# Performance work log

Hardware: AMD Instinct MI355X
Metric: run time of the kernel (lower is better)

Reference implementation:

```python
import jax, jax.numpy as jnp
import numpy as np

H, HKV, D = 16, 4, 64
ROPE_BASE = 10000.0
EPS = 1e-6


def _rms_norm(x):
    return x * jax.lax.rsqrt(jnp.mean(x * x, axis=-1, keepdims=True) + EPS)


def _rope_cos_sin(T, dtype):
    inv_freq = 1.0 / (ROPE_BASE ** (jnp.arange(0, D, 2, dtype=jnp.float32) / D))  # [D/2]
    t = jnp.arange(T, dtype=jnp.float32)
    freqs = jnp.outer(t, inv_freq)  # [T, D/2]
    return jnp.cos(freqs)[None, :, None, :].astype(dtype), jnp.sin(freqs)[None, :, None, :].astype(dtype)


def _apply_rope(x, cos, sin):
    d = x.shape[-1] // 2
    x1, x2 = x[..., :d], x[..., d:]
    return jnp.concatenate([x1 * cos + x2 * sin, -x1 * sin + x2 * cos], axis=-1)


def setup_inputs() -> dict:
    key = jax.random.key(0)
    ks = jax.random.split(key, 6)
    B, T, dm = 1, 2048, 1024
    x = jax.random.normal(ks[0], (B, T, dm), dtype=jnp.float32)
    q_w = jax.random.normal(ks[1], (H * D, dm), dtype=jnp.float32) * 0.02
    k_w = jax.random.normal(ks[2], (HKV * D, dm), dtype=jnp.float32) * 0.02
    v_w = jax.random.normal(ks[3], (HKV * D, dm), dtype=jnp.float32) * 0.02
    o_w = jax.random.normal(ks[4], (dm, H * D), dtype=jnp.float32) * 0.02
    temp = jnp.ones((H,), dtype=jnp.float32) * np.sqrt(D)  # per-head temperature buffer
    curvature = jnp.asarray(1.0, dtype=jnp.float32)
    return {"x": x, "q_w": q_w, "k_w": k_w, "v_w": v_w, "o_w": o_w, "temp": temp, "curvature": curvature}


def reference(x, q_w, k_w, v_w, o_w, temp, curvature):
    B, T, dm = x.shape
    # projections
    q = (x @ q_w.T).reshape(B, T, H, D)
    k = (x @ k_w.T).reshape(B, T, HKV, D)
    v = (x @ v_w.T).reshape(B, T, HKV, D)
    q, k = _rms_norm(q), _rms_norm(k)
    cos, sin = _rope_cos_sin(T, q.dtype)
    q = _apply_rope(q, cos, sin)
    k = _apply_rope(k, cos, sin)
    # GQA: repeat kv heads
    rep = H // HKV
    k = jnp.repeat(k, rep, axis=2)  # [B,T,H,D]
    v = jnp.repeat(v, rep, axis=2)
    c = curvature
    # hyperboloid lift: time component x0 = sqrt(1/c + ||x||^2)
    q0 = jnp.sqrt(1.0 / c + jnp.sum(q * q, axis=-1))  # [B,T,H]
    k0 = jnp.sqrt(1.0 / c + jnp.sum(k * k, axis=-1))
    # Minkowski inner product <q,k>_L = q.k_spatial - q0*k0  -> [B,H,Tq,Tk]
    mink = jnp.einsum('bqhd,bkhd->bhqk', q, k) - q0.transpose(0, 2, 1)[..., :, None] * k0.transpose(0, 2, 1)[..., None, :]
    # Lorentz distance d = arccosh(clamp(-c*<q,k>_L, 1+eps)) / sqrt(c)
    dist = jnp.arccosh(jnp.maximum(-c * mink, 1.0 + 1e-5)) / jnp.sqrt(c)
    scores = -dist / temp[None, :, None, None]
    causal = jnp.tril(jnp.ones((T, T), dtype=bool))
    scores = jnp.where(causal[None, None], scores, -jnp.inf)
    w = jax.nn.softmax(scores, axis=-1)  # [B,H,Tq,Tk]
    attn = jnp.einsum('bhqk,bkhd->bqhd', w, v).reshape(B, T, H * D)
    out = attn @ o_w.T  # [B,T,dm]
    spatial_norm = jnp.mean(jnp.sqrt(jnp.sum(q * q, axis=-1)))
    return out, spatial_norm
```

## Files before the change

kernel.cpp:

```cpp
#include <hip/hip_runtime.h>
#include <hip/hip_bf16.h>

typedef __attribute__((ext_vector_type(8))) short short8;
typedef __attribute__((ext_vector_type(4))) short bf16x4;
typedef __attribute__((ext_vector_type(4))) float f32x4;

#define TT 2048
#define DM 1024
#define NH 16
#define NKV 4
#define HD 64

#define MFMA32(a,b,c) __builtin_amdgcn_mfma_f32_16x16x32_bf16(a,b,c,0,0,0)
#define MFMA16(a,b,c) __builtin_amdgcn_mfma_f32_16x16x16bf16_1k(a,b,c,0,0,0)

__device__ __forceinline__ unsigned short f2bf(float x){
  unsigned int u = __float_as_uint(x);
  u += 0x7fffu + ((u >> 16) & 1u);
  return (unsigned short)(u >> 16);
}
__device__ __forceinline__ unsigned int pkbf2(float x, float y){
  union { __hip_bfloat162 h; unsigned int u; } t;
  t.h = __float22bfloat162_rn(make_float2(x, y));
  return t.u;
}
__device__ __forceinline__ void gl_lds16(const unsigned short* g, unsigned short* l){
  __builtin_amdgcn_global_load_lds(
      (__attribute__((address_space(1))) void*)g,
      (__attribute__((address_space(3))) void*)l, 16, 0, 0);
}

__global__ __launch_bounds__(256) void convertw_kernel(
    const float* __restrict__ x,
    const float* __restrict__ qw, const float* __restrict__ kw,
    const float* __restrict__ vw, const float* __restrict__ ow,
    unsigned short* __restrict__ xb,
    unsigned short* __restrict__ wqkv, unsigned short* __restrict__ owb){
  long v = (long)blockIdx.x * 256 + threadIdx.x;
  const float* src; unsigned short* dst; long base;
  if      (v < 524288) { src = x;  dst = xb;             base = v; }
  else if (v < 786432) { src = qw; dst = wqkv;           base = v - 524288; }
  else if (v < 851968) { src = kw; dst = wqkv + 1048576; base = v - 786432; }
  else if (v < 917504) { src = vw; dst = wqkv + 1310720; base = v - 851968; }
  else                 { src = ow; dst = owb;            base = v - 917504; }
  f32x4 d = *(const f32x4*)(src + base * 4);
  uint2 pk = { pkbf2(d[0], d[1]), pkbf2(d[2], d[3]) };
  *(uint2*)(dst + base * 4) = pk;
}

__global__ __launch_bounds__(256) void gemm1_fused(
    const unsigned short* __restrict__ xb, const unsigned short* __restrict__ wqkv,
    unsigned short* __restrict__ qb, unsigned short* __restrict__ kb,
    unsigned short* __restrict__ vt,
    float* __restrict__ q0, float* __restrict__ k0,
    float* __restrict__ bpart, const float* __restrict__ curv){
  __shared__ __align__(16) unsigned short As[2 * 64 * 32];
  __shared__ __align__(16) unsigned short Bs[2 * 64 * 32];
  __shared__ float Ct[64 * 65];
  __shared__ float bsum;
  const int tid = threadIdx.x, lane = tid & 63, wave = tid >> 6;
  const int hIdx = blockIdx.x;
  const int bm = blockIdx.y * 64, bn = hIdx * 64;
  const int wm = (wave >> 1) * 32, wn = (wave & 1) * 32;
  const int ml = lane & 15, quad = lane >> 4;
  if (tid == 0) bsum = 0.f;
  f32x4 acc[2][2];
  const f32x4 z = {0.f, 0.f, 0.f, 0.f};
  acc[0][0] = z; acc[0][1] = z; acc[1][0] = z; acc[1][1] = z;

  const int srow = wave * 16 + (lane >> 2), scol = (lane & 3) * 8;
  const unsigned short* Ag = xb   + (long)(bm + srow) * 1024 + scol;
  const unsigned short* Bg = wqkv + (long)(bn + srow) * 1024 + scol;
  unsigned short* Al0 = As + wave * 512;
  unsigned short* Al1 = As + 2048 + wave * 512;
  unsigned short* Bl0 = Bs + wave * 512;
  unsigned short* Bl1 = Bs + 2048 + wave * 512;

  for (int kk = 0; kk < 1024; kk += 64){
    __syncthreads();
    gl_lds16(Ag + kk,      Al0);
    gl_lds16(Ag + kk + 32, Al1);
    gl_lds16(Bg + kk,      Bl0);
    gl_lds16(Bg + kk + 32, Bl1);
    __syncthreads();
#pragma unroll
    for (int half = 0; half < 2; half++){
      const unsigned short* Ah = As + half * 2048;
      const unsigned short* Bh = Bs + half * 2048;
      short8 a0f = *(const short8*)&Ah[(wm + ml) * 32 + quad * 8];
      short8 a1f = *(const short8*)&Ah[(wm + 16 + ml) * 32 + quad * 8];
      short8 b0f = *(const short8*)&Bh[(wn + ml) * 32 + quad * 8];
      short8 b1f = *(const short8*)&Bh[(wn + 16 + ml) * 32 + quad * 8];
      acc[0][0] = MFMA32(a0f, b0f, acc[0][0]);
      acc[0][1] = MFMA32(a0f, b1f, acc[0][1]);
      acc[1][0] = MFMA32(a1f, b0f, acc[1][0]);
      acc[1][1] = MFMA32(a1f, b1f, acc[1][1]);
    }
  }
  __syncthreads();
#pragma unroll
  for (int i = 0; i < 2; i++)
#pragma unroll
    for (int j = 0; j < 2; j++)
#pragma unroll
      for (int r = 0; r < 4; r++)
        Ct[(wm + i * 16 + quad * 4 + r) * 65 + wn + j * 16 + ml] = acc[i][j][r];
  __syncthreads();

  if (hIdx < 20){
    const bool isq = hIdx < 16;
    const int h = isq ? hIdx : hIdx - 16;
    const float c = curv[0];
    unsigned short* ob = isq ? qb : kb;
    float* o0 = isq ? q0 : k0;
#pragma unroll 1
    for (int rr = 0; rr < 16; rr++){
      const int row = wave * 16 + rr;
      const int t = bm + row;
      float val = Ct[row * 65 + lane];
      float ss = val * val;
#pragma unroll
      for (int off = 1; off < 64; off <<= 1) ss += __shfl_xor(ss, off);
      float scale = __builtin_amdgcn_rsqf(ss * (1.f / 64.f) + 1e-6f);
      float xn = val * scale;
      float other = __shfl_xor(xn, 32);
      int fi = lane & 31;
      float ang = (float)t * __builtin_amdgcn_exp2f((float)fi * (-13.287712379549449f / 32.f));
      float sn, cs; __sincosf(ang, &sn, &cs);
      float outv = (lane < 32) ? (xn * cs + other * sn) : (xn * cs - other * sn);
      ob[((long)h * TT + t) * 64 + lane] = f2bf(outv);
      if (lane == 0){
        float sq = ss * scale * scale;
        o0[h * TT + t] = __builtin_amdgcn_sqrtf(1.f / c + sq);
        if (isq) atomicAdd(&bsum, __builtin_amdgcn_sqrtf(sq));
      }
    }
  } else {
    const int hk = hIdx - 20;
    const int d = tid >> 2, tseg = (tid & 3) * 16;
    uint4 w0, w1;
    w0.x = pkbf2(Ct[(tseg + 0) * 65 + d], Ct[(tseg + 1) * 65 + d]);
    w0.y = pkbf2(Ct[(tseg + 2) * 65 + d], Ct[(tseg + 3) * 65 + d]);
    w0.z = pkbf2(Ct[(tseg + 4) * 65 + d], Ct[(tseg + 5) * 65 + d]);
    w0.w = pkbf2(Ct[(tseg + 6) * 65 + d], Ct[(tseg + 7) * 65 + d]);
    w1.x = pkbf2(Ct[(tseg + 8) * 65 + d], Ct[(tseg + 9) * 65 + d]);
    w1.y = pkbf2(Ct[(tseg +10) * 65 + d], Ct[(tseg +11) * 65 + d]);
    w1.z = pkbf2(Ct[(tseg +12) * 65 + d], Ct[(tseg +13) * 65 + d]);
    w1.w = pkbf2(Ct[(tseg +14) * 65 + d], Ct[(tseg +15) * 65 + d]);
    const int tile = (bm + tseg) >> 4;
    unsigned short* dst = vt + ((long)(hk * 128 + tile) * 64 + d) * 16;
    *(uint4*)dst = w0;
    *(uint4*)(dst + 8) = w1;
  }
  __syncthreads();
  if (tid == 0) bpart[blockIdx.y * 24 + hIdx] = bsum;
}

__global__ __launch_bounds__(256, 3) void attn_kernel(
    const unsigned short* __restrict__ qb_, const unsigned short* __restrict__ kb_,
    const unsigned short* __restrict__ vt_,
    const float* __restrict__ q0_, const float* __restrict__ k0_,
    const float* __restrict__ temp, const float* __restrict__ curv,
    unsigned short* __restrict__ attn_out,
    const float* __restrict__ bpart, float* __restrict__ out_scalar){
  __shared__ float lds[8 * 1104];
  const int tid = threadIdx.x, lane = tid & 63, wave = tid >> 6;
  const int qt  = 127 - (blockIdx.x >> 3);
  const int sub = blockIdx.x & 7;
  const int kvh = sub >> 1, hp = sub & 1;
  const int h0 = kvh * 4 + hp * 2, h1 = h0 + 1;
  const int i0 = qt * 16;
  const int ml = lane & 15, quad = lane >> 4;
  const float c = curv[0];
  const float rsc = __builtin_amdgcn_rsqf(c);
  const float fac0 = -rsc / temp[h0];
  const float fac1 = -rsc / temp[h1];
  const f32x4 z = {0.f, 0.f, 0.f, 0.f};
  const unsigned short* kh = kb_ + (long)kvh * TT * 64;
  const unsigned short* vh = vt_ + (long)kvh * 128 * 1024;
  const float* k0h = k0_ + kvh * TT;

  short8 qa0 = *(const short8*)&qb_[((long)h0 * TT + i0 + ml) * 64 + quad * 8];
  short8 qa1 = *(const short8*)&qb_[((long)h0 * TT + i0 + ml) * 64 + 32 + quad * 8];
  short8 qb0 = *(const short8*)&qb_[((long)h1 * TT + i0 + ml) * 64 + quad * 8];
  short8 qb1 = *(const short8*)&qb_[((long)h1 * TT + i0 + ml) * 64 + 32 + quad * 8];
  const float q0c0 = c * q0_[h0 * TT + i0 + ml];
  const float q0c1 = c * q0_[h1 * TT + i0 + ml];
  const int rowq = i0 + ml;

  f32x4 o0[4], o1[4];
#pragma unroll
  for (int dt = 0; dt < 4; dt++){ o0[dt] = z; o1[dt] = z; }
  float l0 = 0.f, l1 = 0.f;

  const int nt = (i0 + 47) >> 5;

#pragma unroll 1
  for (int t = wave; t < nt; t += 4){
    const int j0 = t << 5;
    const unsigned short* kp = kh + (long)j0 * 64;
    short8 ka0 = *(const short8*)(kp + ml * 64 + quad * 8);
    short8 ka1 = *(const short8*)(kp + ml * 64 + 32 + quad * 8);
    short8 kc0 = *(const short8*)(kp + (16 + ml) * 64 + quad * 8);
    short8 kc1 = *(const short8*)(kp + (16 + ml) * 64 + 32 + quad * 8);
    f32x4 k0a = *(const f32x4*)(k0h + j0 + quad * 4);
    f32x4 k0b = *(const f32x4*)(k0h + j0 + 16 + quad * 4);
    const unsigned short* vpa = vh + (long)(j0 >> 4) * 1024;
    bf16x4 vfa0 = *(const bf16x4*)(vpa + ( 0 + ml) * 16 + quad * 4);
    bf16x4 vfa1 = *(const bf16x4*)(vpa + (16 + ml) * 16 + quad * 4);
    bf16x4 vfa2 = *(const bf16x4*)(vpa + (32 + ml) * 16 + quad * 4);
    bf16x4 vfa3 = *(const bf16x4*)(vpa + (48 + ml) * 16 + quad * 4);
    bf16x4 vfb0 = *(const bf16x4*)(vpa + 1024 + ( 0 + ml) * 16 + quad * 4);
    bf16x4 vfb1 = *(const bf16x4*)(vpa + 1024 + (16 + ml) * 16 + quad * 4);
    bf16x4 vfb2 = *(const bf16x4*)(vpa + 1024 + (32 + ml) * 16 + quad * 4);
    bf16x4 vfb3 = *(const bf16x4*)(vpa + 1024 + (48 + ml) * 16 + quad * 4);

    const int keyb = j0 + quad * 4;
    const bool nm = (j0 + 31 > i0);
    {
      f32x4 s0 = z, s1 = z;
      s0 = MFMA32(ka0, qa0, s0);
      s0 = MFMA32(ka1, qa1, s0);
      s1 = MFMA32(kc0, qa0, s1);
      s1 = MFMA32(kc1, qa1, s1);
      float p0[4], p1[4];
#pragma unroll
      for (int r = 0; r < 4; r++){
        float argA = fmaxf(__builtin_fmaf(-c, s0[r], q0c0 * k0a[r]), 1.00001f);
        float wA   = argA + __builtin_amdgcn_sqrtf(__builtin_fmaf(argA, argA, -1.f));
        float pA   = __builtin_amdgcn_exp2f(fac0 * __builtin_amdgcn_logf(wA));
        float argB = fmaxf(__builtin_fmaf(-c, s1[r], q0c0 * k0b[r]), 1.00001f);
        float wB   = argB + __builtin_amdgcn_sqrtf(__builtin_fmaf(argB, argB, -1.f));
        float pB   = __builtin_amdgcn_exp2f(fac0 * __builtin_amdgcn_logf(wB));
        if (nm){
          if (keyb + r > rowq)      pA = 0.f;
          if (keyb + 16 + r > rowq) pB = 0.f;
        }
        p0[r] = pA; p1[r] = pB;
        l0 += pA + pB;
      }
      uint2 pua = { pkbf2(p0[0], p0[1]), pkbf2(p0[2], p0[3]) };
      uint2 pub = { pkbf2(p1[0], p1[1]), pkbf2(p1[2], p1[3]) };
      bf16x4 pfa = *(bf16x4*)&pua;
      bf16x4 pfb = *(bf16x4*)&pub;
      o0[0] = MFMA16(vfa0, pfa, o0[0]);
      o0[1] = MFMA16(vfa1, pfa, o0[1]);
      o0[2] = MFMA16(vfa2, pfa, o0[2]);
      o0[3] = MFMA16(vfa3, pfa, o0[3]);
      o0[0] = MFMA16(vfb0, pfb, o0[0]);
      o0[1] = MFMA16(vfb1, pfb, o0[1]);
      o0[2] = MFMA16(vfb2, pfb, o0[2]);
      o0[3] = MFMA16(vfb3, pfb, o0[3]);
    }
    {
      f32x4 s0 = z, s1 = z;
      s0 = MFMA32(ka0, qb0, s0);
      s0 = MFMA32(ka1, qb1, s0);
      s1 = MFMA32(kc0, qb0, s1);
      s1 = MFMA32(kc1, qb1, s1);
      float p0[4], p1[4];
#pragma unroll
      for (int r = 0; r < 4; r++){
        float argA = fmaxf(__builtin_fmaf(-c, s0[r], q0c1 * k0a[r]), 1.00001f);
        float wA   = argA + __builtin_amdgcn_sqrtf(__builtin_fmaf(argA, argA, -1.f));
        float pA   = __builtin_amdgcn_exp2f(fac1 * __builtin_amdgcn_logf(wA));
        float argB = fmaxf(__builtin_fmaf(-c, s1[r], q0c1 * k0b[r]), 1.00001f);
        float wB   = argB + __builtin_amdgcn_sqrtf(__builtin_fmaf(argB, argB, -1.f));
        float pB   = __builtin_amdgcn_exp2f(fac1 * __builtin_amdgcn_logf(wB));
        if (nm){
          if (keyb + r > rowq)      pA = 0.f;
          if (keyb + 16 + r > rowq) pB = 0.f;
        }
        p0[r] = pA; p1[r] = pB;
        l1 += pA + pB;
      }
      uint2 pua = { pkbf2(p0[0], p0[1]), pkbf2(p0[2], p0[3]) };
      uint2 pub = { pkbf2(p1[0], p1[1]), pkbf2(p1[2], p1[3]) };
      bf16x4 pfa = *(bf16x4*)&pua;
      bf16x4 pfb = *(bf16x4*)&pub;
      o1[0] = MFMA16(vfa0, pfa, o1[0]);
      o1[1] = MFMA16(vfa1, pfa, o1[1]);
      o1[2] = MFMA16(vfa2, pfa, o1[2]);
      o1[3] = MFMA16(vfa3, pfa, o1[3]);
      o1[0] = MFMA16(vfb0, pfb, o1[0]);
      o1[1] = MFMA16(vfb1, pfb, o1[1]);
      o1[2] = MFMA16(vfb2, pfb, o1[2]);
      o1[3] = MFMA16(vfb3, pfb, o1[3]);
    }
  }
  l0 += __shfl_xor(l0, 16); l0 += __shfl_xor(l0, 32);
  l1 += __shfl_xor(l1, 16); l1 += __shfl_xor(l1, 32);
  {
    float* w0 = lds + wave * 1104;
    float* w1 = lds + (4 + wave) * 1104;
#pragma unroll
    for (int dt = 0; dt < 4; dt++){
      *(f32x4*)&w0[ml * 68 + dt * 16 + quad * 4] = o0[dt];
      *(f32x4*)&w1[ml * 68 + dt * 16 + quad * 4] = o1[dt];
    }
    if (quad == 0){ w0[1088 + ml] = l0; w1[1088 + ml] = l1; }
  }
  __syncthreads();
  {
    const int row = tid >> 4, c0 = (tid & 15) * 4;
#pragma unroll 1
    for (int hb = 0; hb < 2; hb++){
      const float* base = lds + hb * 4 * 1104;
      float L = 0.f; f32x4 s = z;
#pragma unroll
      for (int w = 0; w < 4; w++){
        const float* rg = base + w * 1104;
        L += rg[1088 + row];
        f32x4 t2 = *(const f32x4*)&rg[row * 68 + c0];
        s[0] += t2[0]; s[1] += t2[1]; s[2] += t2[2]; s[3] += t2[3];
      }
      float invL = __builtin_amdgcn_rcpf(L);
      const int h = hb ? h1 : h0;
      uint2 o = { pkbf2(s[0] * invL, s[1] * invL), pkbf2(s[2] * invL, s[3] * invL) };
      *(uint2*)&attn_out[(long)(i0 + row) * 1024 + h * 64 + c0] = o;
    }
  }
  if (blockIdx.x == 0 && tid < 64){
    float s = 0.f;
    for (int i = lane; i < 768; i += 64) s += bpart[i];
#pragma unroll
    for (int off = 1; off < 64; off <<= 1) s += __shfl_xor(s, off);
    if (lane == 0) out_scalar[0] = s * (1.f / 32768.f);
  }
}

__global__ __launch_bounds__(256) void gemm2_kernel(
    const unsigned short* __restrict__ A, const unsigned short* __restrict__ B,
    float* __restrict__ C){
  __shared__ __align__(16) unsigned short As[2 * 64 * 32];
  __shared__ __align__(16) unsigned short Bs[2 * 64 * 32];
  const int tid = threadIdx.x, lane = tid & 63, wave = tid >> 6;
  const int bm = blockIdx.y * 64, bn = blockIdx.x * 64;
  const int wm = (wave >> 1) * 32, wn = (wave & 1) * 32;
  const int ml = lane & 15, quad = lane >> 4;
  f32x4 acc[2][2];
  const f32x4 z = {0.f, 0.f, 0.f, 0.f};
  acc[0][0] = z; acc[0][1] = z; acc[1][0] = z; acc[1][1] = z;

  const int srow = wave * 16 + (lane >> 2), scol = (lane & 3) * 8;
  const unsigned short* Ag = A + (long)(bm + srow) * 1024 + scol;
  const unsigned short* Bg = B + (long)(bn + srow) * 1024 + scol;
  unsigned short* Al0 = As + wave * 512;
  unsigned short* Al1 = As + 2048 + wave * 512;
  unsigned short* Bl0 = Bs + wave * 512;
  unsigned short* Bl1 = Bs + 2048 + wave * 512;

  for (int kk = 0; kk < 1024; kk += 64){
    __syncthreads();
    gl_lds16(Ag + kk,      Al0);
    gl_lds16(Ag + kk + 32, Al1);
    gl_lds16(Bg + kk,      Bl0);
    gl_lds16(Bg + kk + 32, Bl1);
    __syncthreads();
#pragma unroll
    for (int half = 0; half < 2; half++){
      const unsigned short* Ah = As + half * 2048;
      const unsigned short* Bh = Bs + half * 2048;
      short8 a0f = *(const short8*)&Ah[(wm + ml) * 32 + quad * 8];
      short8 a1f = *(const short8*)&Ah[(wm + 16 + ml) * 32 + quad * 8];
      short8 b0f = *(const short8*)&Bh[(wn + ml) * 32 + quad * 8];
      short8 b1f = *(const short8*)&Bh[(wn + 16 + ml) * 32 + quad * 8];
      acc[0][0] = MFMA32(a0f, b0f, acc[0][0]);
      acc[0][1] = MFMA32(a0f, b1f, acc[0][1]);
      acc[1][0] = MFMA32(a1f, b0f, acc[1][0]);
      acc[1][1] = MFMA32(a1f, b1f, acc[1][1]);
    }
  }
#pragma unroll
  for (int i = 0; i < 2; i++)
#pragma unroll
    for (int j = 0; j < 2; j++)
#pragma unroll
      for (int r = 0; r < 4; r++)
        C[(long)(bm + wm + i * 16 + quad * 4 + r) * 1024 + bn + wn + j * 16 + ml] = acc[i][j][r];
}

extern "C" void kernel_launch(void* const* d_in, const int* in_sizes, int n_in,
                              void* d_out, int out_size, void* d_ws, size_t ws_size,
                              hipStream_t stream){
  const float* x    = (const float*)d_in[0];
  const float* qw   = (const float*)d_in[1];
  const float* kw   = (const float*)d_in[2];
  const float* vw   = (const float*)d_in[3];
  const float* ow   = (const float*)d_in[4];
  const float* temp = (const float*)d_in[5];
  const float* curv = (const float*)d_in[6];
  float* out = (float*)d_out;

  char* ws = (char*)d_ws;
  size_t off = 0;
  auto alloc = [&](size_t bytes) -> char* {
    char* p = ws + off;
    off += (bytes + 255) & ~(size_t)255;
    return p;
  };
  unsigned short* xb   = (unsigned short*)alloc((size_t)TT * DM * 2);
  unsigned short* wqkv = (unsigned short*)alloc((size_t)1536 * DM * 2);
  unsigned short* owb  = (unsigned short*)alloc((size_t)DM * DM * 2);
  unsigned short* qb   = (unsigned short*)alloc((size_t)NH * TT * HD * 2);
  unsigned short* kb   = (unsigned short*)alloc((size_t)NKV * TT * HD * 2);
  unsigned short* vt   = (unsigned short*)alloc((size_t)NKV * TT * HD * 2);
  float*          q0   = (float*)alloc((size_t)NH * TT * 4);
  float*          k0   = (float*)alloc((size_t)NKV * TT * 4);
  unsigned short* attn = (unsigned short*)alloc((size_t)TT * DM * 2);
  float*          bpart= (float*)alloc((size_t)768 * 4);

  convertw_kernel<<<4608, 256, 0, stream>>>(x, qw, kw, vw, ow, xb, wqkv, owb);
  gemm1_fused<<<dim3(24, 32), 256, 0, stream>>>(xb, wqkv, qb, kb, vt, q0, k0, bpart, curv);
  attn_kernel<<<1024, 256, 0, stream>>>(qb, kb, vt, q0, k0, temp, curv, attn,
                                        bpart, out + (size_t)TT * DM);
  gemm2_kernel<<<dim3(16, 32), 256, 0, stream>>>(attn, owb, out);
}
```

Measured before the change: 144.5 us.

## Enlarge GEMM block tiles to 128x64 and alias epilogue LDS with staging buffers

Both projection GEMMs now compute a 128x64 output tile per block, with each wave owning 32 rows by 64 columns (2x4 MFMA accumulators) instead of a 32x32 quadrant. The aim is more MFMA work per LDS fragment load and fewer blocks, which halves the grid, reduces reloading of the B tile, and raises arithmetic intensity. In gemm1 the epilogue transpose buffer shares LDS with the operand staging buffers so the larger tile fits. The trade-off is fewer blocks (384 and 256) across the GPU's compute units and more registers per thread, with the partial-sum buffer for the scalar norm resized to match.

```diff
diff --git a/kernel.cpp b/kernel.cpp
--- a/kernel.cpp
+++ b/kernel.cpp
@@ -54,57 +54,67 @@
     unsigned short* __restrict__ vt,
     float* __restrict__ q0, float* __restrict__ k0,
     float* __restrict__ bpart, const float* __restrict__ curv){
-  __shared__ __align__(16) unsigned short As[2 * 64 * 32];
-  __shared__ __align__(16) unsigned short Bs[2 * 64 * 32];
-  __shared__ float Ct[64 * 65];
+  __shared__ __align__(16) char smem[33280];
+  unsigned short* As = (unsigned short*)smem;
+  unsigned short* Bs = As + 8192;
+  float* Ct = (float*)smem;
   __shared__ float bsum;
   const int tid = threadIdx.x, lane = tid & 63, wave = tid >> 6;
   const int hIdx = blockIdx.x;
-  const int bm = blockIdx.y * 64, bn = hIdx * 64;
-  const int wm = (wave >> 1) * 32, wn = (wave & 1) * 32;
+  const int bm = blockIdx.y * 128, bn = hIdx * 64;
+  const int wm = wave * 32;
   const int ml = lane & 15, quad = lane >> 4;
   if (tid == 0) bsum = 0.f;
-  f32x4 acc[2][2];
+  f32x4 acc[2][4];
   const f32x4 z = {0.f, 0.f, 0.f, 0.f};
-  acc[0][0] = z; acc[0][1] = z; acc[1][0] = z; acc[1][1] = z;
-
-  const int srow = wave * 16 + (lane >> 2), scol = (lane & 3) * 8;
-  const unsigned short* Ag = xb   + (long)(bm + srow) * 1024 + scol;
-  const unsigned short* Bg = wqkv + (long)(bn + srow) * 1024 + scol;
-  unsigned short* Al0 = As + wave * 512;
-  unsigned short* Al1 = As + 2048 + wave * 512;
-  unsigned short* Bl0 = Bs + wave * 512;
-  unsigned short* Bl1 = Bs + 2048 + wave * 512;
+#pragma unroll
+  for (int i = 0; i < 2; i++)
+#pragma unroll
+    for (int j = 0; j < 4; j++) acc[i][j] = z;
+
+  const int lrow = lane >> 2, lcol = (lane & 3) * 8;
+  const unsigned short* AgW = xb   + (long)(bm + wm + lrow) * 1024 + lcol;
+  const unsigned short* BgW = wqkv + (long)(bn + wave * 16 + lrow) * 1024 + lcol;
+  unsigned short* AdW = As + wave * 1024;
+  unsigned short* BdW = Bs + wave * 512;
 
   for (int kk = 0; kk < 1024; kk += 64){
     __syncthreads();
-    gl_lds16(Ag + kk,      Al0);
-    gl_lds16(Ag + kk + 32, Al1);
-    gl_lds16(Bg + kk,      Bl0);
-    gl_lds16(Bg + kk + 32, Bl1);
+#pragma unroll
+    for (int h = 0; h < 2; h++){
+      gl_lds16(AgW + kk + h * 32,            AdW + h * 4096);
+      gl_lds16(AgW + 16384 + kk + h * 32,    AdW + h * 4096 + 512);
+      gl_lds16(BgW + kk + h * 32,            BdW + h * 2048);
+    }
     __syncthreads();
 #pragma unroll
-    for (int half = 0; half < 2; half++){
-      const unsigned short* Ah = As + half * 2048;
-      const unsigned short* Bh = Bs + half * 2048;
+    for (int h = 0; h < 2; h++){
+      const unsigned short* Ah = As + h * 4096;
+      const unsigned short* Bh = Bs + h * 2048;
       short8 a0f = *(const short8*)&Ah[(wm + ml) * 32 + quad * 8];
       short8 a1f = *(const short8*)&Ah[(wm + 16 + ml) * 32 + quad * 8];
-      short8 b0f = *(const short8*)&Bh[(wn + ml) * 32 + quad * 8];
-      short8 b1f = *(const short8*)&Bh[(wn + 16 + ml) * 32 + quad * 8];
+      short8 b0f = *(const short8*)&Bh[(     ml) * 32 + quad * 8];
+      short8 b1f = *(const short8*)&Bh[(16 + ml) * 32 + quad * 8];
+      short8 b2f = *(const short8*)&Bh[(32 + ml) * 32 + quad * 8];
+      short8 b3f = *(const short8*)&Bh[(48 + ml) * 32 + quad * 8];
       acc[0][0] = MFMA32(a0f, b0f, acc[0][0]);
       acc[0][1] = MFMA32(a0f, b1f, acc[0][1]);
+      acc[0][2] = MFMA32(a0f, b2f, acc[0][2]);
+      acc[0][3] = MFMA32(a0f, b3f, acc[0][3]);
       acc[1][0] = MFMA32(a1f, b0f, acc[1][0]);
       acc[1][1] = MFMA32(a1f, b1f, acc[1][1]);
+      acc[1][2] = MFMA32(a1f, b2f, acc[1][2]);
+      acc[1][3] = MFMA32(a1f, b3f, acc[1][3]);
     }
   }
   __syncthreads();
 #pragma unroll
   for (int i = 0; i < 2; i++)
 #pragma unroll
-    for (int j = 0; j < 2; j++)
+    for (int j = 0; j < 4; j++)
 #pragma unroll
       for (int r = 0; r < 4; r++)
-        Ct[(wm + i * 16 + quad * 4 + r) * 65 + wn + j * 16 + ml] = acc[i][j][r];
+        Ct[(wm + i * 16 + quad * 4 + r) * 65 + j * 16 + ml] = acc[i][j][r];
   __syncthreads();
 
   if (hIdx < 20){
@@ -114,8 +124,8 @@
     unsigned short* ob = isq ? qb : kb;
     float* o0 = isq ? q0 : k0;
 #pragma unroll 1
-    for (int rr = 0; rr < 16; rr++){
-      const int row = wave * 16 + rr;
+    for (int rr = 0; rr < 32; rr++){
+      const int row = wave * 32 + rr;
       const int t = bm + row;
       float val = Ct[row * 65 + lane];
       float ss = val * val;
@@ -137,20 +147,24 @@
     }
   } else {
     const int hk = hIdx - 20;
-    const int d = tid >> 2, tseg = (tid & 3) * 16;
-    uint4 w0, w1;
-    w0.x = pkbf2(Ct[(tseg + 0) * 65 + d], Ct[(tseg + 1) * 65 + d]);
-    w0.y = pkbf2(Ct[(tseg + 2) * 65 + d], Ct[(tseg + 3) * 65 + d]);
-    w0.z = pkbf2(Ct[(tseg + 4) * 65 + d], Ct[(tseg + 5) * 65 + d]);
-    w0.w = pkbf2(Ct[(tseg + 6) * 65 + d], Ct[(tseg + 7) * 65 + d]);
-    w1.x = pkbf2(Ct[(tseg + 8) * 65 + d], Ct[(tseg + 9) * 65 + d]);
-    w1.y = pkbf2(Ct[(tseg +10) * 65 + d], Ct[(tseg +11) * 65 + d]);
-    w1.z = pkbf2(Ct[(tseg +12) * 65 + d], Ct[(tseg +13) * 65 + d]);
-    w1.w = pkbf2(Ct[(tseg +14) * 65 + d], Ct[(tseg +15) * 65 + d]);
-    const int tile = (bm + tseg) >> 4;
-    unsigned short* dst = vt + ((long)(hk * 128 + tile) * 64 + d) * 16;
-    *(uint4*)dst = w0;
-    *(uint4*)(dst + 8) = w1;
+    const int d = tid >> 2;
+#pragma unroll
+    for (int half = 0; half < 2; half++){
+      const int tseg = (tid & 3) * 16 + half * 64;
+      uint4 w0, w1;
+      w0.x = pkbf2(Ct[(tseg + 0) * 65 + d], Ct[(tseg + 1) * 65 + d]);
+      w0.y = pkbf2(Ct[(tseg + 2) * 65 + d], Ct[(tseg + 3) * 65 + d]);
+      w0.z = pkbf2(Ct[(tseg + 4) * 65 + d], Ct[(tseg + 5) * 65 + d]);
+      w0.w = pkbf2(Ct[(tseg + 6) * 65 + d], Ct[(tseg + 7) * 65 + d]);
+      w1.x = pkbf2(Ct[(tseg + 8) * 65 + d], Ct[(tseg + 9) * 65 + d]);
+      w1.y = pkbf2(Ct[(tseg +10) * 65 + d], Ct[(tseg +11) * 65 + d]);
+      w1.z = pkbf2(Ct[(tseg +12) * 65 + d], Ct[(tseg +13) * 65 + d]);
+      w1.w = pkbf2(Ct[(tseg +14) * 65 + d], Ct[(tseg +15) * 65 + d]);
+      const int tile = (bm + tseg) >> 4;
+      unsigned short* dst = vt + ((long)(hk * 128 + tile) * 64 + d) * 16;
+      *(uint4*)dst = w0;
+      *(uint4*)(dst + 8) = w1;
+    }
   }
   __syncthreads();
   if (tid == 0) bpart[blockIdx.y * 24 + hIdx] = bsum;
@@ -322,7 +336,7 @@
   }
   if (blockIdx.x == 0 && tid < 64){
     float s = 0.f;
-    for (int i = lane; i < 768; i += 64) s += bpart[i];
+    for (int i = lane; i < 384; i += 64) s += bpart[i];
 #pragma unroll
     for (int off = 1; off < 64; off <<= 1) s += __shfl_xor(s, off);
     if (lane == 0) out_scalar[0] = s * (1.f / 32768.f);
@@ -332,52 +346,61 @@
 __global__ __launch_bounds__(256) void gemm2_kernel(
     const unsigned short* __restrict__ A, const unsigned short* __restrict__ B,
     float* __restrict__ C){
-  __shared__ __align__(16) unsigned short As[2 * 64 * 32];
+  __shared__ __align__(16) unsigned short As[2 * 128 * 32];
   __shared__ __align__(16) unsigned short Bs[2 * 64 * 32];
   const int tid = threadIdx.x, lane = tid & 63, wave = tid >> 6;
-  const int bm = blockIdx.y * 64, bn = blockIdx.x * 64;
-  const int wm = (wave >> 1) * 32, wn = (wave & 1) * 32;
+  const int bm = blockIdx.y * 128, bn = blockIdx.x * 64;
+  const int wm = wave * 32;
   const int ml = lane & 15, quad = lane >> 4;
-  f32x4 acc[2][2];
+  f32x4 acc[2][4];
   const f32x4 z = {0.f, 0.f, 0.f, 0.f};
-  acc[0][0] = z; acc[0][1] = z; acc[1][0] = z; acc[1][1] = z;
-
-  const int srow = wave * 16 + (lane >> 2), scol = (lane & 3) * 8;
-  const unsigned short* Ag = A + (long)(bm + srow) * 1024 + scol;
-  const unsigned short* Bg = B + (long)(bn + srow) * 1024 + scol;
-  unsigned short* Al0 = As + wave * 512;
-  unsigned short* Al1 = As + 2048 + wave * 512;
-  unsigned short* Bl0 = Bs + wave * 512;
-  unsigned short* Bl1 = Bs + 2048 + wave * 512;
+#pragma unroll
+  for (int i = 0; i < 2; i++)
+#pragma unroll
+    for (int j = 0; j < 4; j++) acc[i][j] = z;
+
+  const int lrow = lane >> 2, lcol = (lane & 3) * 8;
+  const unsigned short* AgW = A + (long)(bm + wm + lrow) * 1024 + lcol;
+  const unsigned short* BgW = B + (long)(bn + wave * 16 + lrow) * 1024 + lcol;
+  unsigned short* AdW = As + wave * 1024;
+  unsigned short* BdW = Bs + wave * 512;
 
   for (int kk = 0; kk < 1024; kk += 64){
     __syncthreads();
-    gl_lds16(Ag + kk,      Al0);
-    gl_lds16(Ag + kk + 32, Al1);
-    gl_lds16(Bg + kk,      Bl0);
-    gl_lds16(Bg + kk + 32, Bl1);
+#pragma unroll
+    for (int h = 0; h < 2; h++){
+      gl_lds16(AgW + kk + h * 32,         AdW + h * 4096);
+      gl_lds16(AgW + 16384 + kk + h * 32, AdW + h * 4096 + 512);
+      gl_lds16(BgW + kk + h * 32,         BdW + h * 2048);
+    }
     __syncthreads();
 #pragma unroll
-    for (int half = 0; half < 2; half++){
-      const unsigned short* Ah = As + half * 2048;
-      const unsigned short* Bh = Bs + half * 2048;
+    for (int h = 0; h < 2; h++){
+      const unsigned short* Ah = As + h * 4096;
+      const unsigned short* Bh = Bs + h * 2048;
       short8 a0f = *(const short8*)&Ah[(wm + ml) * 32 + quad * 8];
       short8 a1f = *(const short8*)&Ah[(wm + 16 + ml) * 32 + quad * 8];
-      short8 b0f = *(const short8*)&Bh[(wn + ml) * 32 + quad * 8];
-      short8 b1f = *(const short8*)&Bh[(wn + 16 + ml) * 32 + quad * 8];
+      short8 b0f = *(const short8*)&Bh[(     ml) * 32 + quad * 8];
+      short8 b1f = *(const short8*)&Bh[(16 + ml) * 32 + quad * 8];
+      short8 b2f = *(const short8*)&Bh[(32 + ml) * 32 + quad * 8];
+      short8 b3f = *(const short8*)&Bh[(48 + ml) * 32 + quad * 8];
       acc[0][0] = MFMA32(a0f, b0f, acc[0][0]);
       acc[0][1] = MFMA32(a0f, b1f, acc[0][1]);
+      acc[0][2] = MFMA32(a0f, b2f, acc[0][2]);
+      acc[0][3] = MFMA32(a0f, b3f, acc[0][3]);
       acc[1][0] = MFMA32(a1f, b0f, acc[1][0]);
       acc[1][1] = MFMA32(a1f, b1f, acc[1][1]);
+      acc[1][2] = MFMA32(a1f, b2f, acc[1][2]);
+      acc[1][3] = MFMA32(a1f, b3f, acc[1][3]);
     }
   }
 #pragma unroll
   for (int i = 0; i < 2; i++)
 #pragma unroll
-    for (int j = 0; j < 2; j++)
+    for (int j = 0; j < 4; j++)
 #pragma unroll
       for (int r = 0; r < 4; r++)
-        C[(long)(bm + wm + i * 16 + quad * 4 + r) * 1024 + bn + wn + j * 16 + ml] = acc[i][j][r];
+        C[(long)(bm + wm + i * 16 + quad * 4 + r) * 1024 + bn + j * 16 + ml] = acc[i][j][r];
 }
 
 extern "C" void kernel_launch(void* const* d_in, const int* in_sizes, int n_in,
@@ -408,11 +431,11 @@
   float*          q0   = (float*)alloc((size_t)NH * TT * 4);
   float*          k0   = (float*)alloc((size_t)NKV * TT * 4);
   unsigned short* attn = (unsigned short*)alloc((size_t)TT * DM * 2);
-  float*          bpart= (float*)alloc((size_t)768 * 4);
+  float*          bpart= (float*)alloc((size_t)384 * 4);
 
   convertw_kernel<<<4608, 256, 0, stream>>>(x, qw, kw, vw, ow, xb, wqkv, owb);
-  gemm1_fused<<<dim3(24, 32), 256, 0, stream>>>(xb, wqkv, qb, kb, vt, q0, k0, bpart, curv);
+  gemm1_fused<<<dim3(24, 16), 256, 0, stream>>>(xb, wqkv, qb, kb, vt, q0, k0, bpart, curv);
   attn_kernel<<<1024, 256, 0, stream>>>(qb, kb, vt, q0, k0, temp, curv, attn,
                                         bpart, out + (size_t)TT * DM);
-  gemm2_kernel<<<dim3(16, 32), 256, 0, stream>>>(attn, owb, out);
-}
+  gemm2_kernel<<<dim3(16, 16), 256, 0, stream>>>(attn, owb, out);
+}
```

Result: slower. 155.9 us (+7.9%).
